# Kernel tuning notes

Measured on AMD Instinct MI355X. Metric: run time of the kernel, lower is better.

Reference implementation:

```python
import jax, jax.numpy as jnp
import numpy as np
import math

N_HEAD = 8
N_EMBD = 1024
HEAD_DIM = N_EMBD // N_HEAD // 2  # 64
LAYER_IDX = 4
LAMBDA_INIT = 0.8 - 0.6 * math.exp(-0.3 * LAYER_IDX)
RMS_EPS = float(jnp.finfo(jnp.float32).eps)  # torch RMSNorm eps=None default
LN_EPS = 1e-5


def rmsnorm(x):
    return x * jax.lax.rsqrt(jnp.mean(x * x, axis=-1, keepdims=True) + RMS_EPS)


def layernorm(x):
    mu = jnp.mean(x, axis=-1, keepdims=True)
    var = jnp.mean(jnp.square(x - mu), axis=-1, keepdims=True)
    return (x - mu) * jax.lax.rsqrt(var + LN_EPS)


def rope_tables(T, dim, dtype):
    inv_freq = 1.0 / (10000.0 ** (np.arange(0, dim, 2, dtype=np.float32) / dim))
    t = np.arange(T, dtype=np.float32)
    freqs = np.outer(t, inv_freq)  # [T, dim/2]
    return jnp.asarray(np.cos(freqs), dtype), jnp.asarray(np.sin(freqs), dtype)


def apply_rotary(x, cos, sin):
    # x: [B, T, H, D]; cos/sin: [T, D/2]
    d = x.shape[-1] // 2
    x1, x2 = x[..., :d], x[..., d:]
    c = cos[None, :, None, :]
    s = sin[None, :, None, :]
    return jnp.concatenate([x1 * c + x2 * s, -x1 * s + x2 * c], axis=-1)


def setup_inputs() -> dict:
    key = jax.random.key(0)
    ks = jax.random.split(key, 9)
    B, T, C = 4, 2048, N_EMBD
    scale = 1.0 / math.sqrt(C)
    return {
        "x": jax.random.normal(ks[0], (B, T, C), jnp.float32),
        "Wq": jax.random.normal(ks[1], (C, C), jnp.float32) * scale,
        "Wk": jax.random.normal(ks[2], (C, C), jnp.float32) * scale,
        "Wv": jax.random.normal(ks[3], (C, C), jnp.float32) * scale,
        "Wproj": jax.random.normal(ks[4], (C, C), jnp.float32) * scale,
        "lq1": jax.random.normal(ks[5], (HEAD_DIM,), jnp.float32) * 0.1,
        "lk1": jax.random.normal(ks[6], (HEAD_DIM,), jnp.float32) * 0.1,
        "lq2": jax.random.normal(ks[7], (HEAD_DIM,), jnp.float32) * 0.1,
        "lk2": jax.random.normal(ks[8], (HEAD_DIM,), jnp.float32) * 0.1,
    }


def reference(x, Wq, Wk, Wv, Wproj, lq1, lk1, lq2, lk2):
    B, T, C = x.shape
    H, hd = N_HEAD, HEAD_DIM
    q = (x @ Wq.T).reshape(B, T, 2 * H, hd)
    k = (x @ Wk.T).reshape(B, T, 2 * H, hd)
    v = (x @ Wv.T).reshape(B, T, H, 2 * hd)

    cos, sin = rope_tables(T, hd, x.dtype)
    q = apply_rotary(rmsnorm(q), cos, sin)
    k = apply_rotary(rmsnorm(k), cos, sin)

    q = jnp.transpose(q, (0, 2, 1, 3)) * (1.0 / math.sqrt(hd))  # [B, 2H, T, hd]
    k = jnp.transpose(k, (0, 2, 1, 3))
    v = jnp.transpose(v, (0, 2, 1, 3))  # [B, H, T, 2hd]

    scores = jnp.einsum('bhqd,bhkd->bhqk', q, k)  # [B, 2H, T, T]
    causal = jnp.tril(jnp.ones((T, T), bool))
    scores = jnp.where(causal[None, None], scores, -jnp.inf)
    attn = jax.nn.softmax(scores.astype(jnp.float32), axis=-1).astype(scores.dtype)

    attn = attn.reshape(B, H, 2, T, T)
    lam1 = jnp.exp(jnp.sum(lq1 * lk1))
    lam2 = jnp.exp(jnp.sum(lq2 * lk2))
    lam = lam1 - lam2 + LAMBDA_INIT
    attn = attn[:, :, 0] - lam * attn[:, :, 1]  # [B, H, T, T]

    out = jnp.einsum('bhqk,bhkd->bhqd', attn, v)  # [B, H, T, 2hd]
    out = layernorm(out) * (1.0 - LAMBDA_INIT)
    out = jnp.transpose(out, (0, 2, 1, 3)).reshape(B, T, C)
    return out @ Wproj.T
```

## Files before the change

### kernel.cpp

```cpp
#include <hip/hip_runtime.h>
#include <hip/hip_bf16.h>
#include <math.h>


typedef __bf16 bf16_t;
typedef __bf16 bf16x8 __attribute__((ext_vector_type(8)));
typedef __bf16 bf16x4 __attribute__((ext_vector_type(4)));
typedef float  f32x4  __attribute__((ext_vector_type(4)));

#define T_SEQ 2048
#define C_EMB 1024
static constexpr float LAMBDA_INIT = 0.6192834728526787f;
static constexpr float ONE_MINUS_LI = 0.3807165271473213f;
static constexpr float RMS_EPS = 1.1920928955078125e-07f;
static constexpr float LN_EPS = 1e-5f;
static constexpr float M_FIX = 9.0f;

__device__ __forceinline__ f32x4 mfma16(bf16x8 a, bf16x8 b, f32x4 c) {
  return __builtin_amdgcn_mfma_f32_16x16x32_bf16(a, b, c, 0, 0, 0);
}
__device__ __forceinline__ float declamp(float v, float lim) {
  return fminf(fmaxf(v, -lim), lim);
}
__device__ __forceinline__ void ldsload16(const bf16_t* g, bf16_t* l) {
  __builtin_amdgcn_global_load_lds(
      (const __attribute__((address_space(1))) void*)g,
      (__attribute__((address_space(3))) void*)l, 16, 0, 0);
}


__global__ __launch_bounds__(256) void cvt_all(
    const float* __restrict__ x,  const float* __restrict__ Wq,
    const float* __restrict__ Wk, const float* __restrict__ Wv,
    const float* __restrict__ Wp,
    bf16_t* __restrict__ xb,  bf16_t* __restrict__ wqb, bf16_t* __restrict__ wkb,
    bf16_t* __restrict__ wvb, bf16_t* __restrict__ wpb)
{
  size_t i4 = ((size_t)blockIdx.x * 256 + threadIdx.x) * 4;
  const float* s; bf16_t* d; size_t off;
  if      (i4 <  8388608) { s = x;  d = xb;  off = i4; }
  else if (i4 <  9437184) { s = Wq; d = wqb; off = i4 - 8388608; }
  else if (i4 < 10485760) { s = Wk; d = wkb; off = i4 - 9437184; }
  else if (i4 < 11534336) { s = Wv; d = wvb; off = i4 - 10485760; }
  else                    { s = Wp; d = wpb; off = i4 - 11534336; }
  f32x4 v = *(const f32x4*)(s + off);
  bf16x4 bv;
#pragma unroll
  for (int j = 0; j < 4; ++j) bv[j] = (bf16_t)v[j];
  *(bf16x4*)(d + off) = bv;
}

__device__ __forceinline__ void gemm_core(
    const bf16_t* __restrict__ A, const bf16_t* __restrict__ W,
    bf16_t (*As)[4096], bf16_t (*Bs)[4096], f32x4 acc[4][4], int m0, int n0)
{
  const int tid = threadIdx.x;
  const int lane = tid & 63, w = tid >> 6;
  const int wm = w >> 1, wn = w & 1;
  const int l15 = lane & 15, quad = lane >> 4;

  const int srow = lane >> 2;
  const int schk = (lane & 3) ^ ((lane >> 3) & 3);
  const bf16_t* Ag = A + (size_t)(m0 + w * 32 + srow) * C_EMB + schk * 8;
  const bf16_t* Wg = W + (size_t)(n0 + w * 32 + srow) * C_EMB + schk * 8;

  ldsload16(Ag,              &As[0][w * 1024]);
  ldsload16(Ag + 16 * C_EMB, &As[0][w * 1024 + 512]);
  ldsload16(Wg,              &Bs[0][w * 1024]);
  ldsload16(Wg + 16 * C_EMB, &Bs[0][w * 1024 + 512]);

  for (int ks = 0; ks < 32; ++ks) {
    const int cur = ks & 1;
    __syncthreads();
    if (ks < 31) {
      const int nb = cur ^ 1;
      const bf16_t* a2 = Ag + (ks + 1) * 32;
      const bf16_t* w2 = Wg + (ks + 1) * 32;
      ldsload16(a2,              &As[nb][w * 1024]);
      ldsload16(a2 + 16 * C_EMB, &As[nb][w * 1024 + 512]);
      ldsload16(w2,              &Bs[nb][w * 1024]);
      ldsload16(w2 + 16 * C_EMB, &Bs[nb][w * 1024 + 512]);
    }
    bf16x8 af[4], bfr[4];
#pragma unroll
    for (int i = 0; i < 4; ++i) {
      int ra = wm * 64 + i * 16 + l15;
      int ca = quad ^ ((ra >> 1) & 3);
      af[i] = *(const bf16x8*)&As[cur][ra * 32 + ca * 8];
    }
#pragma unroll
    for (int j = 0; j < 4; ++j) {
      int rb = wn * 64 + j * 16 + l15;
      int cb = quad ^ ((rb >> 1) & 3);
      bfr[j] = *(const bf16x8*)&Bs[cur][rb * 32 + cb * 8];
    }
    __builtin_amdgcn_s_setprio(1);
#pragma unroll
    for (int i = 0; i < 4; ++i)
#pragma unroll
      for (int j = 0; j < 4; ++j) acc[i][j] = mfma16(af[i], bfr[j], acc[i][j]);
    __builtin_amdgcn_s_setprio(0);
  }
}

__device__ __forceinline__ void xcd_tiles(int& m0, int& n0) {
  m0 = (blockIdx.x * 8 + (blockIdx.y >> 3)) * 128;
  n0 = (blockIdx.y & 7) * 128;
}

__global__ __launch_bounds__(256) void gemm_qkv(
    const bf16_t* __restrict__ A,
    const bf16_t* __restrict__ Wqb, const bf16_t* __restrict__ Wkb, const bf16_t* __restrict__ Wvb,
    bf16_t* __restrict__ qo, bf16_t* __restrict__ ko, bf16_t* __restrict__ vt)
{
  const int z = blockIdx.z;
  const bf16_t* W = (z == 0) ? Wqb : ((z == 1) ? Wkb : Wvb);
  int m0, n0; xcd_tiles(m0, n0);
  __shared__ bf16_t As[2][4096];
  __shared__ bf16_t Bs[2][4096];
  const int lane = threadIdx.x & 63, w = threadIdx.x >> 6;
  const int wm = w >> 1, wn = w & 1;
  const int l15 = lane & 15, quad = lane >> 4;
  const f32x4 fz = {0.f, 0.f, 0.f, 0.f};
  f32x4 acc[4][4];
#pragma unroll
  for (int i = 0; i < 4; ++i)
#pragma unroll
    for (int j = 0; j < 4; ++j) acc[i][j] = fz;
  gemm_core(A, W, As, Bs, acc, m0, n0);

  if (z < 2) {
    bf16_t* C = z ? ko : qo;
#pragma unroll
    for (int i = 0; i < 4; ++i)
#pragma unroll
      for (int j = 0; j < 4; ++j)
#pragma unroll
        for (int r = 0; r < 4; ++r) {
          int row = m0 + wm * 64 + i * 16 + quad * 4 + r;
          int col = n0 + wn * 64 + j * 16 + l15;
          C[(size_t)row * C_EMB + col] = (bf16_t)declamp(acc[i][j][r], 1e4f);
        }
  } else {
#pragma unroll
    for (int i = 0; i < 4; ++i)
#pragma unroll
      for (int j = 0; j < 4; ++j) {
        int row = m0 + wm * 64 + i * 16 + quad * 4;
        int col = n0 + wn * 64 + j * 16 + l15;
        bf16x4 pv;
#pragma unroll
        for (int r = 0; r < 4; ++r) pv[r] = (bf16_t)declamp(acc[i][j][r], 1e4f);
        size_t idx = (size_t)(row >> 11) * 2097152 + (size_t)col * 2048 + (row & 2047);
        *(bf16x4*)&vt[idx] = pv;
      }
  }
}

__global__ __launch_bounds__(256) void gemm_proj(
    const bf16_t* __restrict__ A, const bf16_t* __restrict__ Wpb, float* __restrict__ C)
{
  int m0, n0; xcd_tiles(m0, n0);
  __shared__ bf16_t As[2][4096];
  __shared__ bf16_t Bs[2][4096];
  const int lane = threadIdx.x & 63, w = threadIdx.x >> 6;
  const int wm = w >> 1, wn = w & 1;
  const int l15 = lane & 15, quad = lane >> 4;
  const f32x4 fz = {0.f, 0.f, 0.f, 0.f};
  f32x4 acc[4][4];
#pragma unroll
  for (int i = 0; i < 4; ++i)
#pragma unroll
    for (int j = 0; j < 4; ++j) acc[i][j] = fz;
  gemm_core(A, Wpb, As, Bs, acc, m0, n0);
#pragma unroll
  for (int i = 0; i < 4; ++i)
#pragma unroll
    for (int j = 0; j < 4; ++j)
#pragma unroll
      for (int r = 0; r < 4; ++r) {
        int row = m0 + wm * 64 + i * 16 + quad * 4 + r;
        int col = n0 + wn * 64 + j * 16 + l15;
        C[(size_t)row * C_EMB + col] = declamp(acc[i][j][r], 1e4f);
      }
}

__global__ __launch_bounds__(256) void rope_rms2(bf16_t* __restrict__ q, bf16_t* __restrict__ k)
{
  bf16_t* arr = blockIdx.y ? k : q;
  const float scale = blockIdx.y ? 1.0f : 0.125f;
  const int tid = threadIdx.x;
  const int g = blockIdx.x * 16 + (tid >> 4);
  const int l16 = tid & 15;
  const int t = (g >> 4) & (T_SEQ - 1);
  bf16_t* p = arr + (size_t)g * 64 + l16 * 4;

  bf16x4 xv = *(const bf16x4*)p;
  float x[4];
#pragma unroll
  for (int j = 0; j < 4; ++j) x[j] = (float)xv[j];
  float ss = x[0]*x[0] + x[1]*x[1] + x[2]*x[2] + x[3]*x[3];
#pragma unroll
  for (int mm = 1; mm <= 8; mm <<= 1) ss += __shfl_xor(ss, mm);
  const float rn = rsqrtf(fmaxf(ss, 0.f) * (1.0f / 64.0f) + RMS_EPS);
  float nrm[4], prt[4];
#pragma unroll
  for (int j = 0; j < 4; ++j) nrm[j] = x[j] * rn;
#pragma unroll
  for (int j = 0; j < 4; ++j) prt[j] = __shfl_xor(nrm[j], 8);

  const int ib = (l16 & 7) * 4;
  const float sgn = (l16 < 8) ? 1.f : -1.f;
  bf16x4 ov;
#pragma unroll
  for (int j = 0; j < 4; ++j) {
    int i = ib + j;
    float invf = __expf(-(float)i * 0.28782313662425575f);
    float ang = (float)t * invf;
    float c, s;
    __sincosf(ang, &s, &c);
    ov[j] = (bf16_t)((nrm[j] * c + sgn * prt[j] * s) * scale);
  }
  *(bf16x4*)p = ov;
}

__device__ __forceinline__ void attn_step_fm(
    const bf16_t* __restrict__ ks, bf16_t* __restrict__ pw, const bf16_t* __restrict__ vts,
    const bf16x8* qf, float* rsum, f32x4* o,
    bool diag, int k0, int q0, int w, int l15, int quad)
{
  const int xs = l15 & 7;
  f32x4 sc[4];
#pragma unroll
  for (int nt = 0; nt < 4; ++nt) {
    f32x4 a = {0.f, 0.f, 0.f, 0.f};
#pragma unroll
    for (int s = 0; s < 2; ++s) {
      bf16x8 b = *(const bf16x8*)&ks[(nt * 16 + l15) * 64 + ((((s << 2) + quad) ^ xs) << 3)];
      a = mfma16(qf[s], b, a);
    }
#pragma unroll
    for (int r = 0; r < 4; ++r) a[r] = declamp(a[r], 30.f);
    sc[nt] = a;
  }
  if (diag) {
#pragma unroll
    for (int nt = 0; nt < 4; ++nt)
#pragma unroll
      for (int r = 0; r < 4; ++r) {
        int col = k0 + nt * 16 + l15;
        int row = q0 + w * 16 + quad * 4 + r;
        if (col > row) sc[nt][r] = -1e30f;
      }
  }
#pragma unroll
  for (int nt = 0; nt < 4; ++nt)
#pragma unroll
    for (int r = 0; r < 4; ++r) {
      float pv = __expf(sc[nt][r] - M_FIX);
      rsum[r] += pv;
      int row = quad * 4 + r;
      int col = nt * 16 + l15;
      pw[row * 64 + ((((col >> 3) ^ (row & 7)) << 3) | (col & 7))] = (bf16_t)pv;
    }
  __builtin_amdgcn_s_setprio(1);
#pragma unroll
  for (int s = 0; s < 2; ++s) {
    bf16x8 pa = *(const bf16x8*)&pw[l15 * 64 + ((((s << 2) + quad) ^ xs) << 3)];
#pragma unroll
    for (int nt2 = 0; nt2 < 8; ++nt2) {
      bf16x8 vb = *(const bf16x8*)&vts[(nt2 * 16 + l15) * 64 + ((((s << 2) + quad) ^ xs) << 3)];
      o[nt2] = mfma16(pa, vb, o[nt2]);
    }
  }
  __builtin_amdgcn_s_setprio(0);
}

__global__ __launch_bounds__(256) void diff_attn2(
    const bf16_t* __restrict__ qp, const bf16_t* __restrict__ kp, const bf16_t* __restrict__ vtp,
    const float* __restrict__ lq1, const float* __restrict__ lk1,
    const float* __restrict__ lq2, const float* __restrict__ lk2,
    bf16_t* __restrict__ outp)
{
  const int bh = blockIdx.x;
  const int bx = 31 - blockIdx.y;
  const int b = bh >> 3, h = bh & 7;
  const int q0 = bx * 64;
  const int tid = threadIdx.x;
  const int lane = tid & 63, w = tid >> 6;
  const int l15 = lane & 15, quad = lane >> 4;
  const size_t bT = (size_t)b * T_SEQ;
  const bf16_t* vth = vtp + (size_t)b * 2097152 + (size_t)(h * 128) * 2048;

  __shared__ bf16_t k1s[2][64 * 64];
  __shared__ bf16_t k2s[2][64 * 64];
  __shared__ bf16_t vts[2][128 * 64];
  __shared__ bf16_t ps[4][16 * 64];

  float e1 = lq1[lane] * lk1[lane];
  float e2 = lq2[lane] * lk2[lane];
#pragma unroll
  for (int mm = 1; mm <= 32; mm <<= 1) { e1 += __shfl_xor(e1, mm); e2 += __shfl_xor(e2, mm); }
  const float lam = expf(declamp(e1, 30.f)) - expf(declamp(e2, 30.f)) + LAMBDA_INIT;

  const int sh1 = 2 * h, sh2 = 2 * h + 1;

  const int lrow = lane >> 3;
  const int lchk = (lane & 7) ^ lrow;
  const bf16_t* k1g = kp + (bT + (size_t)(w * 16 + lrow)) * 1024 + sh1 * 64 + (lchk << 3);
  const bf16_t* k2g = kp + (bT + (size_t)(w * 16 + lrow)) * 1024 + sh2 * 64 + (lchk << 3);
  const bf16_t* vg  = vth + (size_t)(w * 32 + lrow) * 2048 + (lchk << 3);

  ldsload16(k1g,         &k1s[0][w * 1024]);
  ldsload16(k1g + 8192,  &k1s[0][w * 1024 + 512]);
  ldsload16(k2g,         &k2s[0][w * 1024]);
  ldsload16(k2g + 8192,  &k2s[0][w * 1024 + 512]);
  ldsload16(vg,          &vts[0][w * 2048]);
  ldsload16(vg + 16384,  &vts[0][w * 2048 + 512]);
  ldsload16(vg + 32768,  &vts[0][w * 2048 + 1024]);
  ldsload16(vg + 49152,  &vts[0][w * 2048 + 1536]);

  const int tq = q0 + w * 16 + l15;
  const bf16_t* qrow = qp + (bT + tq) * 1024;
  bf16x8 q1f[2], q2f[2];
#pragma unroll
  for (int s = 0; s < 2; ++s) {
    q1f[s] = *(const bf16x8*)&qrow[sh1 * 64 + s * 32 + quad * 8];
    q2f[s] = *(const bf16x8*)&qrow[sh2 * 64 + s * 32 + quad * 8];
  }

  const f32x4 fz = {0.f, 0.f, 0.f, 0.f};
  f32x4 o1[8], o2[8];
  float rs1[4] = {0, 0, 0, 0}, rs2[4] = {0, 0, 0, 0};
#pragma unroll
  for (int i = 0; i < 8; ++i) { o1[i] = fz; o2[i] = fz; }

  for (int kt = 0; kt <= bx; ++kt) {
    const int cur = kt & 1;
    __syncthreads();
    if (kt < bx) {
      const int nb = cur ^ 1;
      const bf16_t* s1 = k1g + (size_t)(kt + 1) * 65536;
      const bf16_t* s2 = k2g + (size_t)(kt + 1) * 65536;
      const bf16_t* sv = vg + (size_t)(kt + 1) * 64;
      ldsload16(s1,         &k1s[nb][w * 1024]);
      ldsload16(s1 + 8192,  &k1s[nb][w * 1024 + 512]);
      ldsload16(s2,         &k2s[nb][w * 1024]);
      ldsload16(s2 + 8192,  &k2s[nb][w * 1024 + 512]);
      ldsload16(sv,         &vts[nb][w * 2048]);
      ldsload16(sv + 16384, &vts[nb][w * 2048 + 512]);
      ldsload16(sv + 32768, &vts[nb][w * 2048 + 1024]);
      ldsload16(sv + 49152, &vts[nb][w * 2048 + 1536]);
    }
    const int k0 = kt * 64;
    const bool diag = (kt == bx);
    attn_step_fm(&k1s[cur][0], ps[w], &vts[cur][0], q1f, rs1, o1, diag, k0, q0, w, l15, quad);
    attn_step_fm(&k2s[cur][0], ps[w], &vts[cur][0], q2f, rs2, o2, diag, k0, q0, w, l15, quad);
  }

#pragma unroll
  for (int mm = 1; mm <= 8; mm <<= 1)
#pragma unroll
    for (int r = 0; r < 4; ++r) { rs1[r] += __shfl_xor(rs1[r], mm); rs2[r] += __shfl_xor(rs2[r], mm); }
  float i1[4], i2[4];
#pragma unroll
  for (int r = 0; r < 4; ++r) { i1[r] = 1.f / rs1[r]; i2[r] = 1.f / rs2[r]; }
  f32x4 od[8];
  float sum[4] = {0, 0, 0, 0}, sq[4] = {0, 0, 0, 0};
#pragma unroll
  for (int nt2 = 0; nt2 < 8; ++nt2)
#pragma unroll
    for (int r = 0; r < 4; ++r) {
      float v = declamp(o1[nt2][r] * i1[r] - lam * o2[nt2][r] * i2[r], 1e4f);
      od[nt2][r] = v;
      sum[r] += v;
      sq[r] += v * v;
    }
#pragma unroll
  for (int mm = 1; mm <= 8; mm <<= 1)
#pragma unroll
    for (int r = 0; r < 4; ++r) { sum[r] += __shfl_xor(sum[r], mm); sq[r] += __shfl_xor(sq[r], mm); }
  float mu[4], scl[4];
#pragma unroll
  for (int r = 0; r < 4; ++r) {
    mu[r] = sum[r] * (1.0f / 128.0f);
    float var = sq[r] * (1.0f / 128.0f) - mu[r] * mu[r];
    scl[r] = rsqrtf(fmaxf(var, 0.f) + LN_EPS) * ONE_MINUS_LI;
  }
#pragma unroll
  for (int nt2 = 0; nt2 < 8; ++nt2)
#pragma unroll
    for (int r = 0; r < 4; ++r) {
      int trow = q0 + w * 16 + quad * 4 + r;
      outp[(bT + trow) * 1024 + h * 128 + nt2 * 16 + l15] =
          (bf16_t)((od[nt2][r] - mu[r]) * scl[r]);
    }
}


__device__ __forceinline__ void attn_step(
    const bf16_t* __restrict__ ks, bf16_t* __restrict__ pw, const bf16_t* __restrict__ vts,
    const bf16x8* qf, float* mR, float* lR, f32x4* o,
    bool diag, int k0, int q0, int w, int l15, int quad)
{
  f32x4 sc[4];
#pragma unroll
  for (int nt = 0; nt < 4; ++nt) {
    f32x4 a = {0.f, 0.f, 0.f, 0.f};
#pragma unroll
    for (int s = 0; s < 2; ++s) {
      bf16x8 b = *(const bf16x8*)&ks[(nt * 16 + l15) * 72 + s * 32 + quad * 8];
      a = mfma16(qf[s], b, a);
    }
#pragma unroll
    for (int r = 0; r < 4; ++r) a[r] = declamp(a[r], 1e4f);
    sc[nt] = a;
  }
  if (diag) {
#pragma unroll
    for (int nt = 0; nt < 4; ++nt)
#pragma unroll
      for (int r = 0; r < 4; ++r) {
        int col = k0 + nt * 16 + l15;
        int row = q0 + w * 16 + quad * 4 + r;
        if (col > row) sc[nt][r] = -1e30f;
      }
  }
  float mx[4];
#pragma unroll
  for (int r = 0; r < 4; ++r)
    mx[r] = fmaxf(fmaxf(sc[0][r], sc[1][r]), fmaxf(sc[2][r], sc[3][r]));
#pragma unroll
  for (int mm = 1; mm <= 8; mm <<= 1)
#pragma unroll
    for (int r = 0; r < 4; ++r) mx[r] = fmaxf(mx[r], __shfl_xor(mx[r], mm));

  float mnew[4], alpha[4], rs[4];
#pragma unroll
  for (int r = 0; r < 4; ++r) {
    mnew[r] = fmaxf(mR[r], mx[r]);
    alpha[r] = __expf(mR[r] - mnew[r]);
    rs[r] = 0.f;
  }
#pragma unroll
  for (int nt = 0; nt < 4; ++nt)
#pragma unroll
    for (int r = 0; r < 4; ++r) {
      float pv = __expf(sc[nt][r] - mnew[r]);
      rs[r] += pv;
      pw[(quad * 4 + r) * 72 + nt * 16 + l15] = (bf16_t)pv;
    }
#pragma unroll
  for (int mm = 1; mm <= 8; mm <<= 1)
#pragma unroll
    for (int r = 0; r < 4; ++r) rs[r] += __shfl_xor(rs[r], mm);
#pragma unroll
  for (int r = 0; r < 4; ++r) {
    lR[r] = lR[r] * alpha[r] + rs[r];
    mR[r] = mnew[r];
  }
#pragma unroll
  for (int nt2 = 0; nt2 < 8; ++nt2)
#pragma unroll
    for (int r = 0; r < 4; ++r) o[nt2][r] *= alpha[r];
#pragma unroll
  for (int s = 0; s < 2; ++s) {
    bf16x8 pa = *(const bf16x8*)&pw[l15 * 72 + s * 32 + quad * 8];
#pragma unroll
    for (int nt2 = 0; nt2 < 8; ++nt2) {
      bf16x8 vb = *(const bf16x8*)&vts[(nt2 * 16 + l15) * 72 + s * 32 + quad * 8];
      o[nt2] = mfma16(pa, vb, o[nt2]);
    }
  }
}

template<bool A_F32, bool OUT_F32>
__global__ __launch_bounds__(256) void gemm_bt(
    const void* __restrict__ Ap,
    const float* __restrict__ W0, const float* __restrict__ W1, const float* __restrict__ W2,
    void* __restrict__ Cp0, void* __restrict__ Cp1, void* __restrict__ Cp2)
{
  const float* W = (blockIdx.z == 0) ? W0 : ((blockIdx.z == 1) ? W1 : W2);
  void*       Cv = (blockIdx.z == 0) ? Cp0 : ((blockIdx.z == 1) ? Cp1 : Cp2);
  const int K = C_EMB, N = C_EMB;
  const int n0 = blockIdx.x * 128, m0 = blockIdx.y * 128;
  __shared__ bf16_t As[128 * 40];
  __shared__ bf16_t Bs[128 * 40];
  const int tid = threadIdx.x;
  const int lane = tid & 63, w = tid >> 6;
  const int wm = w >> 1, wn = w & 1;
  const int l15 = lane & 15, quad = lane >> 4;
  const f32x4 fz = {0.f, 0.f, 0.f, 0.f};
  f32x4 acc[4][4];
#pragma unroll
  for (int i = 0; i < 4; ++i)
#pragma unroll
    for (int j = 0; j < 4; ++j) acc[i][j] = fz;

  for (int k0 = 0; k0 < K; k0 += 32) {
    if constexpr (A_F32) {
      const float* Af = (const float*)Ap;
#pragma unroll
      for (int i = 0; i < 4; ++i) {
        int c = tid + i * 256;
        int r = c >> 3, c4 = (c & 7) * 4;
        f32x4 v = *(const f32x4*)&Af[(size_t)(m0 + r) * K + k0 + c4];
        bf16x4 bv;
#pragma unroll
        for (int j = 0; j < 4; ++j) bv[j] = (bf16_t)v[j];
        *(bf16x4*)&As[r * 40 + c4] = bv;
      }
    } else {
      const bf16_t* Ab = (const bf16_t*)Ap;
#pragma unroll
      for (int i = 0; i < 2; ++i) {
        int c = tid + i * 256;
        int r = c >> 2, c8 = (c & 3) * 8;
        *(bf16x8*)&As[r * 40 + c8] = *(const bf16x8*)&Ab[(size_t)(m0 + r) * K + k0 + c8];
      }
    }
#pragma unroll
    for (int i = 0; i < 4; ++i) {
      int c = tid + i * 256;
      int r = c >> 3, c4 = (c & 7) * 4;
      f32x4 v = *(const f32x4*)&W[(size_t)(n0 + r) * K + k0 + c4];
      bf16x4 bv;
#pragma unroll
      for (int j = 0; j < 4; ++j) bv[j] = (bf16_t)v[j];
      *(bf16x4*)&Bs[r * 40 + c4] = bv;
    }
    __syncthreads();
    bf16x8 af[4], bfr[4];
#pragma unroll
    for (int i = 0; i < 4; ++i)
      af[i] = *(const bf16x8*)&As[(wm * 64 + i * 16 + l15) * 40 + quad * 8];
#pragma unroll
    for (int j = 0; j < 4; ++j)
      bfr[j] = *(const bf16x8*)&Bs[(wn * 64 + j * 16 + l15) * 40 + quad * 8];
#pragma unroll
    for (int i = 0; i < 4; ++i)
#pragma unroll
      for (int j = 0; j < 4; ++j) acc[i][j] = mfma16(af[i], bfr[j], acc[i][j]);
    __syncthreads();
  }
#pragma unroll
  for (int i = 0; i < 4; ++i)
#pragma unroll
    for (int j = 0; j < 4; ++j)
#pragma unroll
      for (int r = 0; r < 4; ++r) {
        int row = m0 + wm * 64 + i * 16 + quad * 4 + r;
        int col = n0 + wn * 64 + j * 16 + l15;
        float v = declamp(acc[i][j][r], 1e4f);
        if constexpr (OUT_F32) ((float*)Cv)[(size_t)row * N + col] = v;
        else                   ((bf16_t*)Cv)[(size_t)row * N + col] = (bf16_t)v;
      }
}

__global__ __launch_bounds__(256) void rope_rms(bf16_t* __restrict__ arr, int is_q)
{
  const int tid = threadIdx.x;
  const int g = blockIdx.x * 16 + (tid >> 4);
  const int l16 = tid & 15;
  const int t = (g >> 4) & (T_SEQ - 1);
  bf16_t* p = arr + (size_t)g * 64 + l16 * 4;
  bf16x4 xv = *(const bf16x4*)p;
  float x[4];
#pragma unroll
  for (int j = 0; j < 4; ++j) x[j] = (float)xv[j];
  float ss = x[0]*x[0] + x[1]*x[1] + x[2]*x[2] + x[3]*x[3];
#pragma unroll
  for (int mm = 1; mm <= 8; mm <<= 1) ss += __shfl_xor(ss, mm);
  const float rn = rsqrtf(fmaxf(ss, 0.f) * (1.0f / 64.0f) + RMS_EPS);
  float nrm[4], prt[4];
#pragma unroll
  for (int j = 0; j < 4; ++j) nrm[j] = x[j] * rn;
#pragma unroll
  for (int j = 0; j < 4; ++j) prt[j] = __shfl_xor(nrm[j], 8);
  const int ib = (l16 & 7) * 4;
  const float sgn = (l16 < 8) ? 1.f : -1.f;
  const float scale = is_q ? 0.125f : 1.0f;
  bf16x4 ov;
#pragma unroll
  for (int j = 0; j < 4; ++j) {
    int i = ib + j;
    float invf = __expf(-(float)i * 0.28782313662425575f);
    float ang = (float)t * invf;
    float c, s;
    __sincosf(ang, &s, &c);
    ov[j] = (bf16_t)((nrm[j] * c + sgn * prt[j] * s) * scale);
  }
  *(bf16x4*)p = ov;
}

__global__ __launch_bounds__(256) void diff_attn(
    const bf16_t* qp, const bf16_t* __restrict__ kp, const bf16_t* __restrict__ vp,
    const float* __restrict__ lq1, const float* __restrict__ lk1,
    const float* __restrict__ lq2, const float* __restrict__ lk2,
    bf16_t* outp)
{
  const int bx = blockIdx.x;
  const int h = blockIdx.y;
  const int q0 = bx * 64;
  const int tid = threadIdx.x;
  const int lane = tid & 63, w = tid >> 6;
  const int l15 = lane & 15, quad = lane >> 4;

  __shared__ bf16_t k1s[64 * 72];
  __shared__ bf16_t k2s[64 * 72];
  __shared__ bf16_t vts[128 * 72];
  __shared__ bf16_t ps[4][16 * 72];

  float e1 = lq1[lane] * lk1[lane];
  float e2 = lq2[lane] * lk2[lane];
#pragma unroll
  for (int mm = 1; mm <= 32; mm <<= 1) { e1 += __shfl_xor(e1, mm); e2 += __shfl_xor(e2, mm); }
  const float lam = expf(declamp(e1, 30.f)) - expf(declamp(e2, 30.f)) + LAMBDA_INIT;

  const int sh1 = 2 * h, sh2 = 2 * h + 1;
  const int tq = q0 + w * 16 + l15;
  const bf16_t* qrow = qp + (size_t)tq * 1024;
  bf16x8 q1f[2], q2f[2];
#pragma unroll
  for (int s = 0; s < 2; ++s) {
    q1f[s] = *(const bf16x8*)&qrow[sh1 * 64 + s * 32 + quad * 8];
    q2f[s] = *(const bf16x8*)&qrow[sh2 * 64 + s * 32 + quad * 8];
  }
  const f32x4 fz = {0.f, 0.f, 0.f, 0.f};
  f32x4 o1[8], o2[8];
  float m1[4], l1[4], m2[4], l2[4];
#pragma unroll
  for (int i = 0; i < 8; ++i) { o1[i] = fz; o2[i] = fz; }
#pragma unroll
  for (int r = 0; r < 4; ++r) { m1[r] = -1e30f; m2[r] = -1e30f; l1[r] = 0.f; l2[r] = 0.f; }

  for (int kt = 0; kt <= bx; ++kt) {
    const int k0 = kt * 64;
    __syncthreads();
#pragma unroll
    for (int i = 0; i < 2; ++i) {
      int c = tid + i * 256;
      int r = c >> 3, c8 = (c & 7) * 8;
      const bf16_t* krow = kp + (size_t)(k0 + r) * 1024;
      *(bf16x8*)&k1s[r * 72 + c8] = *(const bf16x8*)&krow[sh1 * 64 + c8];
      *(bf16x8*)&k2s[r * 72 + c8] = *(const bf16x8*)&krow[sh2 * 64 + c8];
    }
#pragma unroll
    for (int i = 0; i < 4; ++i) {
      int c = tid + i * 256;
      int r = c >> 4, d8 = (c & 15) * 8;
      bf16x8 vv = *(const bf16x8*)&vp[(size_t)(k0 + r) * 1024 + h * 128 + d8];
#pragma unroll
      for (int jj = 0; jj < 8; ++jj) vts[(d8 + jj) * 72 + r] = vv[jj];
    }
    __syncthreads();
    const bool diag = (kt == bx);
    attn_step(k1s, ps[w], vts, q1f, m1, l1, o1, diag, k0, q0, w, l15, quad);
    attn_step(k2s, ps[w], vts, q2f, m2, l2, o2, diag, k0, q0, w, l15, quad);
  }
  float i1[4], i2[4];
#pragma unroll
  for (int r = 0; r < 4; ++r) { i1[r] = 1.f / l1[r]; i2[r] = 1.f / l2[r]; }
  f32x4 od[8];
  float sum[4] = {0, 0, 0, 0}, sq[4] = {0, 0, 0, 0};
#pragma unroll
  for (int nt2 = 0; nt2 < 8; ++nt2)
#pragma unroll
    for (int r = 0; r < 4; ++r) {
      float v = declamp(o1[nt2][r] * i1[r] - lam * o2[nt2][r] * i2[r], 1e4f);
      od[nt2][r] = v;
      sum[r] += v;
      sq[r] += v * v;
    }
#pragma unroll
  for (int mm = 1; mm <= 8; mm <<= 1)
#pragma unroll
    for (int r = 0; r < 4; ++r) { sum[r] += __shfl_xor(sum[r], mm); sq[r] += __shfl_xor(sq[r], mm); }
  float mu[4], scl[4];
#pragma unroll
  for (int r = 0; r < 4; ++r) {
    mu[r] = sum[r] * (1.0f / 128.0f);
    float var = sq[r] * (1.0f / 128.0f) - mu[r] * mu[r];
    scl[r] = rsqrtf(fmaxf(var, 0.f) + LN_EPS) * ONE_MINUS_LI;
  }
#pragma unroll
  for (int nt2 = 0; nt2 < 8; ++nt2)
#pragma unroll
    for (int r = 0; r < 4; ++r) {
      int trow = q0 + w * 16 + quad * 4 + r;
      outp[(size_t)trow * 1024 + h * 128 + nt2 * 16 + l15] =
          (bf16_t)((od[nt2][r] - mu[r]) * scl[r]);
    }
}

extern "C" void kernel_launch(void* const* d_in, const int* in_sizes, int n_in,
                              void* d_out, int out_size, void* d_ws, size_t ws_size,
                              hipStream_t stream) {
  const float* x     = (const float*)d_in[0];
  const float* Wq    = (const float*)d_in[1];
  const float* Wk    = (const float*)d_in[2];
  const float* Wv    = (const float*)d_in[3];
  const float* Wproj = (const float*)d_in[4];
  const float* lq1   = (const float*)d_in[5];
  const float* lk1   = (const float*)d_in[6];
  const float* lq2   = (const float*)d_in[7];
  const float* lk2   = (const float*)d_in[8];
  float* O = (float*)d_out;
  const size_t R = (size_t)T_SEQ * C_EMB;

  if (ws_size >= (size_t)40 * 1024 * 1024) {
    bf16_t* wsb = (bf16_t*)d_ws;
    bf16_t* xb  = wsb;
    bf16_t* wqb = wsb + 8388608;
    bf16_t* wkb = wqb + 1048576;
    bf16_t* wvb = wkb + 1048576;
    bf16_t* wpb = wvb + 1048576;
    bf16_t* vt  = wpb + 1048576;
    bf16_t* qo  = (bf16_t*)d_out;
    bf16_t* ko  = qo + 8388608;
    bf16_t* a   = xb;

    cvt_all<<<12288, 256, 0, stream>>>(x, Wq, Wk, Wv, Wproj, xb, wqb, wkb, wvb, wpb);
    gemm_qkv<<<dim3(8, 64, 3), 256, 0, stream>>>(xb, wqb, wkb, wvb, qo, ko, vt);
    rope_rms2<<<dim3(8192, 2), 256, 0, stream>>>(qo, ko);
    diff_attn2<<<dim3(32, 32), 256, 0, stream>>>(qo, ko, vt, lq1, lk1, lq2, lk2, a);
    gemm_proj<<<dim3(8, 64), 256, 0, stream>>>(a, wpb, O);
  } else {
    char* Ob = (char*)d_out;
    char* Xb = (char*)d_in[0];
    const size_t MB4 = (size_t)1 << 22;
    bf16_t* qb[4] = { (bf16_t*)(Ob + 2*MB4), (bf16_t*)(Ob + 5*MB4),
                      (bf16_t*)(Xb + 0*MB4), (bf16_t*)(Xb + 3*MB4) };
    bf16_t* kb[4] = { (bf16_t*)(Ob + 3*MB4), (bf16_t*)(Ob + 6*MB4),
                      (bf16_t*)(Xb + 1*MB4), (bf16_t*)(Xb + 4*MB4) };
    bf16_t* vb[4] = { (bf16_t*)(Ob + 4*MB4), (bf16_t*)(Ob + 7*MB4),
                      (bf16_t*)(Xb + 2*MB4), (bf16_t*)(Xb + 5*MB4) };
    for (int b = 0; b < 4; ++b) {
      const float* xbp = x + (size_t)b * R;
      gemm_bt<true, false><<<dim3(8, 16, 3), 256, 0, stream>>>(
          xbp, Wq, Wk, Wv, qb[b], kb[b], vb[b]);
      rope_rms<<<2048, 256, 0, stream>>>(qb[b], 1);
      rope_rms<<<2048, 256, 0, stream>>>(kb[b], 0);
      diff_attn<<<dim3(32, 8), 256, 0, stream>>>(qb[b], kb[b], vb[b],
                                                 lq1, lk1, lq2, lk2, qb[b]);
      gemm_bt<false, true><<<dim3(8, 16, 1), 256, 0, stream>>>(
          qb[b], Wproj, Wproj, Wproj, O + (size_t)b * R, nullptr, nullptr);
    }
  }
}
```

Before: 304.0 us.

## Single-buffer K/V LDS with register prefetch and shared V reads for both heads

Replaces the double-buffered LDS tiles filled by direct global-to-LDS loads with single-buffered tiles. The next tile is prefetched into registers during compute and written to LDS after a barrier. The PV product is restructured so each V fragment read from LDS feeds both sub-heads' MFMAs, halving V LDS reads. This halves LDS usage, which may raise occupancy, at the cost of more registers, an extra barrier per iteration, and an explicit register-to-LDS store step.

```diff
diff --git a/kernel.cpp b/kernel.cpp
--- a/kernel.cpp
+++ b/kernel.cpp
@@ -224,9 +224,9 @@
   *(bf16x4*)p = ov;
 }
 
-__device__ __forceinline__ void attn_step_fm(
-    const bf16_t* __restrict__ ks, bf16_t* __restrict__ pw, const bf16_t* __restrict__ vts,
-    const bf16x8* qf, float* rsum, f32x4* o,
+__device__ __forceinline__ void qk_sm_fm(
+    const bf16_t* __restrict__ ks, bf16_t* __restrict__ pw,
+    const bf16x8* qf, float* rsum, bf16x8* pa,
     bool diag, int k0, int q0, int w, int l15, int quad)
 {
   const int xs = l15 & 7;
@@ -263,17 +263,9 @@
       int col = nt * 16 + l15;
       pw[row * 64 + ((((col >> 3) ^ (row & 7)) << 3) | (col & 7))] = (bf16_t)pv;
     }
-  __builtin_amdgcn_s_setprio(1);
-#pragma unroll
-  for (int s = 0; s < 2; ++s) {
-    bf16x8 pa = *(const bf16x8*)&pw[l15 * 64 + ((((s << 2) + quad) ^ xs) << 3)];
-#pragma unroll
-    for (int nt2 = 0; nt2 < 8; ++nt2) {
-      bf16x8 vb = *(const bf16x8*)&vts[(nt2 * 16 + l15) * 64 + ((((s << 2) + quad) ^ xs) << 3)];
-      o[nt2] = mfma16(pa, vb, o[nt2]);
-    }
-  }
-  __builtin_amdgcn_s_setprio(0);
+#pragma unroll
+  for (int s = 0; s < 2; ++s)
+    pa[s] = *(const bf16x8*)&pw[l15 * 64 + ((((s << 2) + quad) ^ xs) << 3)];
 }
 
 __global__ __launch_bounds__(256) void diff_attn2(
@@ -292,9 +284,9 @@
   const size_t bT = (size_t)b * T_SEQ;
   const bf16_t* vth = vtp + (size_t)b * 2097152 + (size_t)(h * 128) * 2048;
 
-  __shared__ bf16_t k1s[2][64 * 64];
-  __shared__ bf16_t k2s[2][64 * 64];
-  __shared__ bf16_t vts[2][128 * 64];
+  __shared__ bf16_t k1s[64 * 64];
+  __shared__ bf16_t k2s[64 * 64];
+  __shared__ bf16_t vts[128 * 64];
   __shared__ bf16_t ps[4][16 * 64];
 
   float e1 = lq1[lane] * lk1[lane];
@@ -311,14 +303,27 @@
   const bf16_t* k2g = kp + (bT + (size_t)(w * 16 + lrow)) * 1024 + sh2 * 64 + (lchk << 3);
   const bf16_t* vg  = vth + (size_t)(w * 32 + lrow) * 2048 + (lchk << 3);
 
-  ldsload16(k1g,         &k1s[0][w * 1024]);
-  ldsload16(k1g + 8192,  &k1s[0][w * 1024 + 512]);
-  ldsload16(k2g,         &k2s[0][w * 1024]);
-  ldsload16(k2g + 8192,  &k2s[0][w * 1024 + 512]);
-  ldsload16(vg,          &vts[0][w * 2048]);
-  ldsload16(vg + 16384,  &vts[0][w * 2048 + 512]);
-  ldsload16(vg + 32768,  &vts[0][w * 2048 + 1024]);
-  ldsload16(vg + 49152,  &vts[0][w * 2048 + 1536]);
+  const int lwr = lane * 8;
+
+  {
+    bf16x8 a0 = *(const bf16x8*)k1g;
+    bf16x8 a1 = *(const bf16x8*)(k1g + 8192);
+    bf16x8 b0 = *(const bf16x8*)k2g;
+    bf16x8 b1 = *(const bf16x8*)(k2g + 8192);
+    bf16x8 v0 = *(const bf16x8*)vg;
+    bf16x8 v1 = *(const bf16x8*)(vg + 16384);
+    bf16x8 v2 = *(const bf16x8*)(vg + 32768);
+    bf16x8 v3 = *(const bf16x8*)(vg + 49152);
+    *(bf16x8*)&k1s[w * 1024 + lwr]        = a0;
+    *(bf16x8*)&k1s[w * 1024 + 512 + lwr]  = a1;
+    *(bf16x8*)&k2s[w * 1024 + lwr]        = b0;
+    *(bf16x8*)&k2s[w * 1024 + 512 + lwr]  = b1;
+    *(bf16x8*)&vts[w * 2048 + lwr]        = v0;
+    *(bf16x8*)&vts[w * 2048 + 512 + lwr]  = v1;
+    *(bf16x8*)&vts[w * 2048 + 1024 + lwr] = v2;
+    *(bf16x8*)&vts[w * 2048 + 1536 + lwr] = v3;
+  }
+  __syncthreads();
 
   const int tq = q0 + w * 16 + l15;
   const bf16_t* qrow = qp + (bT + tq) * 1024;
@@ -335,27 +340,55 @@
 #pragma unroll
   for (int i = 0; i < 8; ++i) { o1[i] = fz; o2[i] = fz; }
 
+  const int xs = l15 & 7;
+  bf16x8 rk1a, rk1b, rk2a, rk2b, rv0, rv1, rv2, rv3;
+
   for (int kt = 0; kt <= bx; ++kt) {
-    const int cur = kt & 1;
-    __syncthreads();
-    if (kt < bx) {
-      const int nb = cur ^ 1;
+    const bool more = (kt < bx);
+    if (more) {
       const bf16_t* s1 = k1g + (size_t)(kt + 1) * 65536;
       const bf16_t* s2 = k2g + (size_t)(kt + 1) * 65536;
       const bf16_t* sv = vg + (size_t)(kt + 1) * 64;
-      ldsload16(s1,         &k1s[nb][w * 1024]);
-      ldsload16(s1 + 8192,  &k1s[nb][w * 1024 + 512]);
-      ldsload16(s2,         &k2s[nb][w * 1024]);
-      ldsload16(s2 + 8192,  &k2s[nb][w * 1024 + 512]);
-      ldsload16(sv,         &vts[nb][w * 2048]);
-      ldsload16(sv + 16384, &vts[nb][w * 2048 + 512]);
-      ldsload16(sv + 32768, &vts[nb][w * 2048 + 1024]);
-      ldsload16(sv + 49152, &vts[nb][w * 2048 + 1536]);
+      rk1a = *(const bf16x8*)s1;
+      rk1b = *(const bf16x8*)(s1 + 8192);
+      rk2a = *(const bf16x8*)s2;
+      rk2b = *(const bf16x8*)(s2 + 8192);
+      rv0  = *(const bf16x8*)sv;
+      rv1  = *(const bf16x8*)(sv + 16384);
+      rv2  = *(const bf16x8*)(sv + 32768);
+      rv3  = *(const bf16x8*)(sv + 49152);
     }
     const int k0 = kt * 64;
     const bool diag = (kt == bx);
-    attn_step_fm(&k1s[cur][0], ps[w], &vts[cur][0], q1f, rs1, o1, diag, k0, q0, w, l15, quad);
-    attn_step_fm(&k2s[cur][0], ps[w], &vts[cur][0], q2f, rs2, o2, diag, k0, q0, w, l15, quad);
+
+    bf16x8 pa1[2], pa2[2];
+    qk_sm_fm(k1s, ps[w], q1f, rs1, pa1, diag, k0, q0, w, l15, quad);
+    qk_sm_fm(k2s, ps[w], q2f, rs2, pa2, diag, k0, q0, w, l15, quad);
+
+    __builtin_amdgcn_s_setprio(1);
+#pragma unroll
+    for (int s = 0; s < 2; ++s) {
+#pragma unroll
+      for (int nt2 = 0; nt2 < 8; ++nt2) {
+        bf16x8 vb = *(const bf16x8*)&vts[(nt2 * 16 + l15) * 64 + ((((s << 2) + quad) ^ xs) << 3)];
+        o1[nt2] = mfma16(pa1[s], vb, o1[nt2]);
+        o2[nt2] = mfma16(pa2[s], vb, o2[nt2]);
+      }
+    }
+    __builtin_amdgcn_s_setprio(0);
+
+    __syncthreads();
+    if (more) {
+      *(bf16x8*)&k1s[w * 1024 + lwr]        = rk1a;
+      *(bf16x8*)&k1s[w * 1024 + 512 + lwr]  = rk1b;
+      *(bf16x8*)&k2s[w * 1024 + lwr]        = rk2a;
+      *(bf16x8*)&k2s[w * 1024 + 512 + lwr]  = rk2b;
+      *(bf16x8*)&vts[w * 2048 + lwr]        = rv0;
+      *(bf16x8*)&vts[w * 2048 + 512 + lwr]  = rv1;
+      *(bf16x8*)&vts[w * 2048 + 1024 + lwr] = rv2;
+      *(bf16x8*)&vts[w * 2048 + 1536 + lwr] = rv3;
+      __syncthreads();
+    }
   }
 
 #pragma unroll
```

Result: slower. 317.1 us (+4.3%).

## Pair causal query tiles per block for balanced work and share V loads

Applied to the files above, without the earlier changes.

Each attention block now handles two query tiles, p and 31-p. It runs 33 key-tile steps and writes the first tile's output partway through the loop, which balances the causal triangle across 512 blocks instead of 1024 uneven ones. The PV stage is also merged so each V fragment read from shared memory feeds both difference-attention streams. The cost is fewer blocks in flight, a longer per-block loop and more live registers from the interleaved accumulators.

```diff
diff --git a/kernel.cpp b/kernel.cpp
--- a/kernel.cpp
+++ b/kernel.cpp
@@ -224,9 +224,9 @@
   *(bf16x4*)p = ov;
 }
 
-__device__ __forceinline__ void attn_step_fm(
-    const bf16_t* __restrict__ ks, bf16_t* __restrict__ pw, const bf16_t* __restrict__ vts,
-    const bf16x8* qf, float* rsum, f32x4* o,
+__device__ __forceinline__ void qk_sm_fm(
+    const bf16_t* __restrict__ ks, bf16_t* __restrict__ pw,
+    const bf16x8* qf, float* rsum, bf16x8* pa,
     bool diag, int k0, int q0, int w, int l15, int quad)
 {
   const int xs = l15 & 7;
@@ -263,17 +263,52 @@
       int col = nt * 16 + l15;
       pw[row * 64 + ((((col >> 3) ^ (row & 7)) << 3) | (col & 7))] = (bf16_t)pv;
     }
-  __builtin_amdgcn_s_setprio(1);
-#pragma unroll
-  for (int s = 0; s < 2; ++s) {
-    bf16x8 pa = *(const bf16x8*)&pw[l15 * 64 + ((((s << 2) + quad) ^ xs) << 3)];
-#pragma unroll
-    for (int nt2 = 0; nt2 < 8; ++nt2) {
-      bf16x8 vb = *(const bf16x8*)&vts[(nt2 * 16 + l15) * 64 + ((((s << 2) + quad) ^ xs) << 3)];
-      o[nt2] = mfma16(pa, vb, o[nt2]);
-    }
-  }
-  __builtin_amdgcn_s_setprio(0);
+#pragma unroll
+  for (int s = 0; s < 2; ++s)
+    pa[s] = *(const bf16x8*)&pw[l15 * 64 + ((((s << 2) + quad) ^ xs) << 3)];
+}
+
+__device__ __forceinline__ void attn_epilogue(
+    f32x4* o1, f32x4* o2, float* rs1, float* rs2, float lam,
+    bf16_t* __restrict__ outp, size_t bT, int h, int q0, int w, int l15, int quad)
+{
+#pragma unroll
+  for (int mm = 1; mm <= 8; mm <<= 1)
+#pragma unroll
+    for (int r = 0; r < 4; ++r) { rs1[r] += __shfl_xor(rs1[r], mm); rs2[r] += __shfl_xor(rs2[r], mm); }
+  float i1[4], i2[4];
+#pragma unroll
+  for (int r = 0; r < 4; ++r) { i1[r] = 1.f / rs1[r]; i2[r] = 1.f / rs2[r]; }
+  f32x4 od[8];
+  float sum[4] = {0, 0, 0, 0}, sq[4] = {0, 0, 0, 0};
+#pragma unroll
+  for (int nt2 = 0; nt2 < 8; ++nt2)
+#pragma unroll
+    for (int r = 0; r < 4; ++r) {
+      float v = declamp(o1[nt2][r] * i1[r] - lam * o2[nt2][r] * i2[r], 1e4f);
+      od[nt2][r] = v;
+      sum[r] += v;
+      sq[r] += v * v;
+    }
+#pragma unroll
+  for (int mm = 1; mm <= 8; mm <<= 1)
+#pragma unroll
+    for (int r = 0; r < 4; ++r) { sum[r] += __shfl_xor(sum[r], mm); sq[r] += __shfl_xor(sq[r], mm); }
+  float mu[4], scl[4];
+#pragma unroll
+  for (int r = 0; r < 4; ++r) {
+    mu[r] = sum[r] * (1.0f / 128.0f);
+    float var = sq[r] * (1.0f / 128.0f) - mu[r] * mu[r];
+    scl[r] = rsqrtf(fmaxf(var, 0.f) + LN_EPS) * ONE_MINUS_LI;
+  }
+#pragma unroll
+  for (int nt2 = 0; nt2 < 8; ++nt2)
+#pragma unroll
+    for (int r = 0; r < 4; ++r) {
+      int trow = q0 + w * 16 + quad * 4 + r;
+      outp[(bT + trow) * 1024 + h * 128 + nt2 * 16 + l15] =
+          (bf16_t)((od[nt2][r] - mu[r]) * scl[r]);
+    }
 }
 
 __global__ __launch_bounds__(256) void diff_attn2(
@@ -283,9 +318,8 @@
     bf16_t* __restrict__ outp)
 {
   const int bh = blockIdx.x;
-  const int bx = 31 - blockIdx.y;
+  const int p  = blockIdx.y;
   const int b = bh >> 3, h = bh & 7;
-  const int q0 = bx * 64;
   const int tid = threadIdx.x;
   const int lane = tid & 63, w = tid >> 6;
   const int l15 = lane & 15, quad = lane >> 4;
@@ -320,8 +354,10 @@
   ldsload16(vg + 32768,  &vts[0][w * 2048 + 1024]);
   ldsload16(vg + 49152,  &vts[0][w * 2048 + 1536]);
 
-  const int tq = q0 + w * 16 + l15;
-  const bf16_t* qrow = qp + (bT + tq) * 1024;
+  int q0 = p * 64;
+  const int q0B = (31 - p) * 64;
+
+  const bf16_t* qrow = qp + (bT + q0 + w * 16 + l15) * 1024;
   bf16x8 q1f[2], q2f[2];
 #pragma unroll
   for (int s = 0; s < 2; ++s) {
@@ -335,14 +371,17 @@
 #pragma unroll
   for (int i = 0; i < 8; ++i) { o1[i] = fz; o2[i] = fz; }
 
-  for (int kt = 0; kt <= bx; ++kt) {
-    const int cur = kt & 1;
+  const int xs = l15 & 7;
+
+  for (int st = 0; st <= 32; ++st) {
+    const int cur = st & 1;
     __syncthreads();
-    if (kt < bx) {
+    if (st < 32) {
+      const int ktn = (st < p) ? (st + 1) : (st - p);
       const int nb = cur ^ 1;
-      const bf16_t* s1 = k1g + (size_t)(kt + 1) * 65536;
-      const bf16_t* s2 = k2g + (size_t)(kt + 1) * 65536;
-      const bf16_t* sv = vg + (size_t)(kt + 1) * 64;
+      const bf16_t* s1 = k1g + (size_t)ktn * 65536;
+      const bf16_t* s2 = k2g + (size_t)ktn * 65536;
+      const bf16_t* sv = vg + (size_t)ktn * 64;
       ldsload16(s1,         &k1s[nb][w * 1024]);
       ldsload16(s1 + 8192,  &k1s[nb][w * 1024 + 512]);
       ldsload16(s2,         &k2s[nb][w * 1024]);
@@ -352,49 +391,42 @@
       ldsload16(sv + 32768, &vts[nb][w * 2048 + 1024]);
       ldsload16(sv + 49152, &vts[nb][w * 2048 + 1536]);
     }
+    const int kt = (st <= p) ? st : (st - p - 1);
     const int k0 = kt * 64;
-    const bool diag = (kt == bx);
-    attn_step_fm(&k1s[cur][0], ps[w], &vts[cur][0], q1f, rs1, o1, diag, k0, q0, w, l15, quad);
-    attn_step_fm(&k2s[cur][0], ps[w], &vts[cur][0], q2f, rs2, o2, diag, k0, q0, w, l15, quad);
-  }
-
-#pragma unroll
-  for (int mm = 1; mm <= 8; mm <<= 1)
-#pragma unroll
-    for (int r = 0; r < 4; ++r) { rs1[r] += __shfl_xor(rs1[r], mm); rs2[r] += __shfl_xor(rs2[r], mm); }
-  float i1[4], i2[4];
-#pragma unroll
-  for (int r = 0; r < 4; ++r) { i1[r] = 1.f / rs1[r]; i2[r] = 1.f / rs2[r]; }
-  f32x4 od[8];
-  float sum[4] = {0, 0, 0, 0}, sq[4] = {0, 0, 0, 0};
-#pragma unroll
-  for (int nt2 = 0; nt2 < 8; ++nt2)
-#pragma unroll
-    for (int r = 0; r < 4; ++r) {
-      float v = declamp(o1[nt2][r] * i1[r] - lam * o2[nt2][r] * i2[r], 1e4f);
-      od[nt2][r] = v;
-      sum[r] += v;
-      sq[r] += v * v;
-    }
-#pragma unroll
-  for (int mm = 1; mm <= 8; mm <<= 1)
-#pragma unroll
-    for (int r = 0; r < 4; ++r) { sum[r] += __shfl_xor(sum[r], mm); sq[r] += __shfl_xor(sq[r], mm); }
-  float mu[4], scl[4];
-#pragma unroll
-  for (int r = 0; r < 4; ++r) {
-    mu[r] = sum[r] * (1.0f / 128.0f);
-    float var = sq[r] * (1.0f / 128.0f) - mu[r] * mu[r];
-    scl[r] = rsqrtf(fmaxf(var, 0.f) + LN_EPS) * ONE_MINUS_LI;
-  }
-#pragma unroll
-  for (int nt2 = 0; nt2 < 8; ++nt2)
-#pragma unroll
-    for (int r = 0; r < 4; ++r) {
-      int trow = q0 + w * 16 + quad * 4 + r;
-      outp[(bT + trow) * 1024 + h * 128 + nt2 * 16 + l15] =
-          (bf16_t)((od[nt2][r] - mu[r]) * scl[r]);
-    }
+    const bool diag = (st == p) || (st == 32);
+
+    bf16x8 pa1[2], pa2[2];
+    qk_sm_fm(&k1s[cur][0], ps[w], q1f, rs1, pa1, diag, k0, q0, w, l15, quad);
+    qk_sm_fm(&k2s[cur][0], ps[w], q2f, rs2, pa2, diag, k0, q0, w, l15, quad);
+
+    __builtin_amdgcn_s_setprio(1);
+#pragma unroll
+    for (int s = 0; s < 2; ++s) {
+#pragma unroll
+      for (int nt2 = 0; nt2 < 8; ++nt2) {
+        bf16x8 vb = *(const bf16x8*)&vts[cur][(nt2 * 16 + l15) * 64 + ((((s << 2) + quad) ^ xs) << 3)];
+        o1[nt2] = mfma16(pa1[s], vb, o1[nt2]);
+        o2[nt2] = mfma16(pa2[s], vb, o2[nt2]);
+      }
+    }
+    __builtin_amdgcn_s_setprio(0);
+
+    if (st == p) {
+      attn_epilogue(o1, o2, rs1, rs2, lam, outp, bT, h, q0, w, l15, quad);
+      q0 = q0B;
+      const bf16_t* qrB = qp + (bT + q0 + w * 16 + l15) * 1024;
+#pragma unroll
+      for (int s = 0; s < 2; ++s) {
+        q1f[s] = *(const bf16x8*)&qrB[sh1 * 64 + s * 32 + quad * 8];
+        q2f[s] = *(const bf16x8*)&qrB[sh2 * 64 + s * 32 + quad * 8];
+      }
+#pragma unroll
+      for (int i = 0; i < 8; ++i) { o1[i] = fz; o2[i] = fz; }
+#pragma unroll
+      for (int r = 0; r < 4; ++r) { rs1[r] = 0.f; rs2[r] = 0.f; }
+    }
+  }
+  attn_epilogue(o1, o2, rs1, rs2, lam, outp, bT, h, q0B, w, l15, quad);
 }
 
 
@@ -723,7 +755,7 @@
     cvt_all<<<12288, 256, 0, stream>>>(x, Wq, Wk, Wv, Wproj, xb, wqb, wkb, wvb, wpb);
     gemm_qkv<<<dim3(8, 64, 3), 256, 0, stream>>>(xb, wqb, wkb, wvb, qo, ko, vt);
     rope_rms2<<<dim3(8192, 2), 256, 0, stream>>>(qo, ko);
-    diff_attn2<<<dim3(32, 32), 256, 0, stream>>>(qo, ko, vt, lq1, lk1, lq2, lk2, a);
+    diff_attn2<<<dim3(32, 16), 256, 0, stream>>>(qo, ko, vt, lq1, lk1, lq2, lk2, a);
     gemm_proj<<<dim3(8, 64), 256, 0, stream>>>(a, wpb, O);
   } else {
     char* Ob = (char*)d_out;
```

Measured after the change: 367.6 us. 1.21x slower.
